# Performance work log

Measured on AMD Instinct MI355X. Metric: run time of the kernel, lower is better.

The kernel has to match this reference:

```python
import jax, jax.numpy as jnp
import numpy as np

N_NODES = 100000
N_EDGES = 1600000
D_IN, D_HID, D_OUT = 128, 128, 40


def _degrees(src, dst, n):
    ones = jnp.ones((src.shape[0],), dtype=jnp.float32)
    out_deg = jax.ops.segment_sum(ones, src, num_segments=n)
    in_deg = jax.ops.segment_sum(ones, dst, num_segments=n)
    # DGL clamps zero degrees to 1 to avoid inf
    return jnp.maximum(out_deg, 1.0), jnp.maximum(in_deg, 1.0)


def _graph_conv(x, W, b, src, dst, out_norm, in_norm, n):
    # norm='both': h = D_in^{-1/2} * A^T * (D_out^{-1/2} * x W) + b
    h = x @ W                      # [N, d_out] (W applied first: d_in >= d_out)
    h = h * out_norm[:, None]      # scale source features
    agg = jax.ops.segment_sum(h[src], dst, num_segments=n)  # gather-scatter SpMM
    return agg * in_norm[:, None] + b


def setup_inputs() -> dict:
    key = jax.random.key(0)
    ks = jax.random.split(key, 8)
    x = jax.random.normal(ks[0], (N_NODES, D_IN), dtype=jnp.float32)
    edge_index = jax.random.randint(ks[1], (2, N_EDGES), 0, N_NODES, dtype=jnp.int32)
    def glorot(k, fan_in, fan_out):
        lim = np.sqrt(6.0 / (fan_in + fan_out)).astype(np.float32)
        return jax.random.uniform(k, (fan_in, fan_out), jnp.float32, -lim, lim)
    return {
        "x": x,
        "edge_index": edge_index,
        "W1": glorot(ks[2], D_IN, D_HID), "b1": jnp.zeros((D_HID,), jnp.float32),
        "W2": glorot(ks[3], D_HID, D_HID), "b2": jnp.zeros((D_HID,), jnp.float32),
        "W3": glorot(ks[4], D_HID, D_OUT), "b3": jnp.zeros((D_OUT,), jnp.float32),
    }


def reference(x, edge_index, W1, b1, W2, b2, W3, b3):
    src, dst = edge_index[0], edge_index[1]
    out_deg, in_deg = _degrees(src, dst, N_NODES)
    out_norm = jax.lax.rsqrt(out_deg)
    in_norm = jax.lax.rsqrt(in_deg)
    h = _graph_conv(x, W1, b1, src, dst, out_norm, in_norm, N_NODES)
    h = jax.nn.relu(h)  # dropout inactive at inference
    h = _graph_conv(h, W2, b2, src, dst, out_norm, in_norm, N_NODES)
    h = jax.nn.relu(h)
    h = _graph_conv(h, W3, b3, src, dst, out_norm, in_norm, N_NODES)
    return jax.nn.log_softmax(h, axis=-1)
```

## Files before the change

kernel.cpp:

```cpp
#include <hip/hip_runtime.h>
#include <hip/hip_bf16.h>
#include <math.h>

typedef __hip_bfloat16 bf16;
typedef __attribute__((ext_vector_type(8))) short short8v;
typedef __attribute__((ext_vector_type(4))) float f32x4;

#define ELLW 64
#define NPB 256
#define NBMAX 512
#define CAPB 8192
#define CHUNKA 4096

__device__ __forceinline__ float bflo(unsigned u) { return __uint_as_float(u << 16); }
__device__ __forceinline__ float bfhi(unsigned u) { return __uint_as_float(u & 0xffff0000u); }
__device__ __forceinline__ unsigned short f2bf(float f) {
    unsigned u = __float_as_uint(f);
    return (unsigned short)((u + 0x7fff + ((u >> 16) & 1)) >> 16);
}


__device__ __forceinline__ void pack_one(const float* __restrict__ W, bf16* __restrict__ Wb,
                                         int idx, int NOUT, int NPAD) {
    int r = idx & 7;
    int rest = idx >> 3;
    int col = rest % NPAD;
    int sk = rest / NPAD;
    int k = sk * 8 + r;
    float v = (col < NOUT) ? W[k * NOUT + col] : 0.0f;
    Wb[idx] = __float2bfloat16(v);
}

__global__ void pack_all(const float* __restrict__ W1, const float* __restrict__ W2,
                         const float* __restrict__ W3, bf16* __restrict__ Wb1,
                         bf16* __restrict__ Wb2, bf16* __restrict__ Wb3) {
    int idx = blockIdx.x * blockDim.x + threadIdx.x;
    if (idx < 16384) pack_one(W1, Wb1, idx, 128, 128);
    else if (idx < 32768) pack_one(W2, Wb2, idx - 16384, 128, 128);
    else if (idx < 40960) pack_one(W3, Wb3, idx - 32768, 40, 64);
}


template <int NT>
__device__ void gemm_body_f32(int bid, const float* __restrict__ Af,
                              const bf16* __restrict__ Wb, bf16* __restrict__ H, int n) {
    constexpr int NPAD = NT * 16;
    int lane = threadIdx.x & 63;
    int wid = threadIdx.x >> 6;
    int base = (bid * 4 + wid) * 16;
    if (base >= n) return;
    int m = lane & 15, kb = lane >> 4;
    int arow = base + m;

    short8v az = {0, 0, 0, 0, 0, 0, 0, 0};
    short8v a[4];
    const float4* apf = (const float4*)(Af + (size_t)arow * 128);
#pragma unroll
    for (int s = 0; s < 4; ++s) {
        short8v w = az;
        if (arow < n) {
            float4 p = apf[s * 8 + kb * 2];
            float4 q = apf[s * 8 + kb * 2 + 1];
            w[0] = (short)f2bf(p.x); w[1] = (short)f2bf(p.y);
            w[2] = (short)f2bf(p.z); w[3] = (short)f2bf(p.w);
            w[4] = (short)f2bf(q.x); w[5] = (short)f2bf(q.y);
            w[6] = (short)f2bf(q.z); w[7] = (short)f2bf(q.w);
        }
        a[s] = w;
    }

    f32x4 zz = {0.f, 0.f, 0.f, 0.f};
    f32x4 acc[NT];
#pragma unroll
    for (int t = 0; t < NT; ++t) acc[t] = zz;

    const short8v* bp = (const short8v*)Wb;
#pragma unroll
    for (int s = 0; s < 4; ++s) {
#pragma unroll
        for (int t = 0; t < NT; ++t) {
            short8v b = bp[(size_t)(s * 4 + kb) * NPAD + t * 16 + m];
            acc[t] = __builtin_amdgcn_mfma_f32_16x16x32_bf16(a[s], b, acc[t], 0, 0, 0);
        }
    }

    int orow0 = base + kb * 4;
#pragma unroll
    for (int r = 0; r < 4; ++r) {
        int rr = orow0 + r;
        if (rr < n) {
#pragma unroll
            for (int t = 0; t < NT; ++t)
                H[(size_t)rr * NPAD + t * 16 + m] = __float2bfloat16(acc[t][r]);
        }
    }
}


__device__ void scatter_body(int bid, const int* __restrict__ src, const int* __restrict__ dst,
                             int nbk, int* __restrict__ gCurD, int* __restrict__ gCurS,
                             unsigned* __restrict__ pairD, int* __restrict__ srcS, int E) {
    __shared__ int histD[NBMAX], histS[NBMAX], offD[NBMAX], offS[NBMAX];
    int tid = threadIdx.x;
    int base = bid * CHUNKA;
    int cnt = E - base; if (cnt > CHUNKA) cnt = CHUNKA;
    for (int i = tid; i < nbk; i += 256) { histD[i] = 0; histS[i] = 0; }
    __syncthreads();
    int sv[16], dv[16];
#pragma unroll
    for (int j = 0; j < 16; ++j) {
        int idx = tid + j * 256;
        if (idx < cnt) {
            sv[j] = src[base + idx];
            dv[j] = dst[base + idx];
            atomicAdd(&histD[dv[j] >> 8], 1);
            atomicAdd(&histS[sv[j] >> 8], 1);
        } else sv[j] = -1;
    }
    __syncthreads();
    for (int i = tid; i < nbk; i += 256) {
        offD[i] = atomicAdd(&gCurD[i], histD[i]);
        offS[i] = atomicAdd(&gCurS[i], histS[i]);
    }
    __syncthreads();
    for (int i = tid; i < nbk; i += 256) { histD[i] = 0; histS[i] = 0; }
    __syncthreads();
#pragma unroll
    for (int j = 0; j < 16; ++j) {
        if (sv[j] >= 0) {
            int bd = dv[j] >> 8;
            int p = atomicAdd(&histD[bd], 1) + offD[bd];
            if (p < CAPB)
                pairD[(size_t)bd * CAPB + p] = ((unsigned)(dv[j] & 255) << 17) | (unsigned)sv[j];
            int bs = sv[j] >> 8;
            int q = atomicAdd(&histS[bs], 1) + offS[bs];
            if (q < CAPB) srcS[(size_t)bs * CAPB + q] = sv[j];
        }
    }
}


__global__ void phase1(const int* __restrict__ src, const int* __restrict__ dst,
                       int nbk, int* __restrict__ gCurD, int* __restrict__ gCurS,
                       unsigned* __restrict__ pairD, int* __restrict__ srcS, int E,
                       int scatterBlocks, const float* __restrict__ x,
                       const bf16* __restrict__ Wb1, bf16* __restrict__ H, int n) {
    if ((int)blockIdx.x < scatterBlocks)
        scatter_body(blockIdx.x, src, dst, nbk, gCurD, gCurS, pairD, srcS, E);
    else
        gemm_body_f32<8>(blockIdx.x - scatterBlocks, x, Wb1, H, n);
}


__global__ void phase2(const unsigned* __restrict__ pairD, const int* __restrict__ srcS,
                       const int* __restrict__ gCurD, const int* __restrict__ gCurS,
                       int* __restrict__ ell, int* __restrict__ cnt_in,
                       float* __restrict__ innf, float* __restrict__ outn, int nbk, int n) {
    int bid = blockIdx.x;
    int tid = threadIdx.x;
    if (bid < nbk) {
        __shared__ int cnt[NPB];
        cnt[tid & (NPB - 1)] = 0;
        __syncthreads();
        int m = gCurD[bid]; if (m > CAPB) m = CAPB;
        const unsigned* p = pairD + (size_t)bid * CAPB;
        int nb0 = bid << 8;
        for (int i = tid; i < m; i += 256) {
            unsigned v = p[i];
            int local = (int)(v >> 17);
            int s = (int)(v & 0x1FFFF);
            int pos = atomicAdd(&cnt[local], 1);
            if (pos < ELLW) ell[((size_t)(nb0 + local) << 6) + pos] = s;
        }
        __syncthreads();
        int node = nb0 + tid;
        if (tid < NPB && node < n) {
            cnt_in[node] = cnt[tid];
            innf[node] = rsqrtf(fmaxf((float)cnt[tid], 1.0f));
        }
    } else {
        int b = bid - nbk;
        __shared__ int cnt2[NPB];
        cnt2[tid & (NPB - 1)] = 0;
        __syncthreads();
        int m = gCurS[b]; if (m > CAPB) m = CAPB;
        const int* p = srcS + (size_t)b * CAPB;
        int nb0 = b << 8;
        for (int i = tid; i < m; i += 256)
            atomicAdd(&cnt2[p[i] - nb0], 1);
        __syncthreads();
        int node = nb0 + tid;
        if (tid < NPB && node < n)
            outn[node] = rsqrtf(fmaxf((float)cnt2[tid], 1.0f));
    }
}


template <int NT>
__global__ void gather_gemm_fused(const bf16* __restrict__ h, const int* __restrict__ cnt_in,
                                  const int* __restrict__ ell, const float* __restrict__ outn,
                                  const float* __restrict__ inn, const float* __restrict__ bias,
                                  const bf16* __restrict__ Wb, bf16* __restrict__ H, int n) {
    constexpr int NPAD = NT * 16;
    constexpr int NTW = NT / 4;
    __shared__ short rows[16][136];
    int lane = threadIdx.x & 63;
    int wid = threadIdx.x >> 6;
    int nodeBase = blockIdx.x * 16;
    const unsigned* hu = (const unsigned*)h;

#pragma unroll
    for (int q = 0; q < 4; ++q) {
        int r = wid * 4 + q;
        int node = nodeBase + r;
        unsigned pk = 0;
        if (node < n) {
            int d = min(cnt_in[node], ELLW);
            const int4* row4 = (const int4*)(ell + ((size_t)node << 6));
            const int* row = (const int*)row4;
            float a0 = 0.f, a1 = 0.f, a2 = 0.f, a3 = 0.f;
            float a4 = 0.f, a5 = 0.f, a6 = 0.f, a7 = 0.f;
            int k = 0;
            for (; k + 7 < d; k += 8) {
                int kq = k >> 2;
                int4 q0 = row4[kq], q1 = row4[kq + 1];
                unsigned u0 = hu[((size_t)q0.x << 6) + lane];
                unsigned u1 = hu[((size_t)q0.y << 6) + lane];
                unsigned u2 = hu[((size_t)q0.z << 6) + lane];
                unsigned u3 = hu[((size_t)q0.w << 6) + lane];
                unsigned u4 = hu[((size_t)q1.x << 6) + lane];
                unsigned u5 = hu[((size_t)q1.y << 6) + lane];
                unsigned u6 = hu[((size_t)q1.z << 6) + lane];
                unsigned u7 = hu[((size_t)q1.w << 6) + lane];
                float o0 = outn[q0.x], o1 = outn[q0.y], o2 = outn[q0.z], o3 = outn[q0.w];
                float o4 = outn[q1.x], o5 = outn[q1.y], o6 = outn[q1.z], o7 = outn[q1.w];
                a0 += o0 * bflo(u0); a1 += o0 * bfhi(u0);
                a2 += o1 * bflo(u1); a3 += o1 * bfhi(u1);
                a4 += o2 * bflo(u2); a5 += o2 * bfhi(u2);
                a6 += o3 * bflo(u3); a7 += o3 * bfhi(u3);
                a0 += o4 * bflo(u4); a1 += o4 * bfhi(u4);
                a2 += o5 * bflo(u5); a3 += o5 * bfhi(u5);
                a4 += o6 * bflo(u6); a5 += o6 * bfhi(u6);
                a6 += o7 * bflo(u7); a7 += o7 * bfhi(u7);
            }
            for (; k + 3 < d; k += 4) {
                int4 q0 = row4[k >> 2];
                unsigned u0 = hu[((size_t)q0.x << 6) + lane];
                unsigned u1 = hu[((size_t)q0.y << 6) + lane];
                unsigned u2 = hu[((size_t)q0.z << 6) + lane];
                unsigned u3 = hu[((size_t)q0.w << 6) + lane];
                float o0 = outn[q0.x], o1 = outn[q0.y], o2 = outn[q0.z], o3 = outn[q0.w];
                a0 += o0 * bflo(u0); a1 += o0 * bfhi(u0);
                a2 += o1 * bflo(u1); a3 += o1 * bfhi(u1);
                a4 += o2 * bflo(u2); a5 += o2 * bfhi(u2);
                a6 += o3 * bflo(u3); a7 += o3 * bfhi(u3);
            }
            for (; k < d; ++k) {
                int e = row[k];
                unsigned u = hu[((size_t)e << 6) + lane];
                float o = outn[e];
                a0 += o * bflo(u); a1 += o * bfhi(u);
            }
            float innv = inn[node];
            float2 bb = ((const float2*)bias)[lane];
            float f0 = fmaxf(((a0 + a2) + (a4 + a6)) * innv + bb.x, 0.0f);
            float f1 = fmaxf(((a1 + a3) + (a5 + a7)) * innv + bb.y, 0.0f);
            pk = (unsigned)f2bf(f0) | ((unsigned)f2bf(f1) << 16);
        }
        ((unsigned*)rows[r])[lane] = pk;
    }
    __syncthreads();

    int m = lane & 15, kb = lane >> 4;
    short8v a[4];
#pragma unroll
    for (int s = 0; s < 4; ++s)
        a[s] = *(const short8v*)&rows[m][s * 32 + kb * 8];

    f32x4 zz = {0.f, 0.f, 0.f, 0.f};
    f32x4 acc[NTW];
#pragma unroll
    for (int t = 0; t < NTW; ++t) acc[t] = zz;

    const short8v* bp = (const short8v*)Wb;
#pragma unroll
    for (int s = 0; s < 4; ++s) {
#pragma unroll
        for (int t = 0; t < NTW; ++t) {
            int tt = wid * NTW + t;
            short8v b = bp[(size_t)(s * 4 + kb) * NPAD + tt * 16 + m];
            acc[t] = __builtin_amdgcn_mfma_f32_16x16x32_bf16(a[s], b, acc[t], 0, 0, 0);
        }
    }

    int orow0 = nodeBase + kb * 4;
#pragma unroll
    for (int r = 0; r < 4; ++r) {
        int rr = orow0 + r;
        if (rr < n) {
#pragma unroll
            for (int t = 0; t < NTW; ++t)
                H[(size_t)rr * NPAD + (wid * NTW + t) * 16 + m] = __float2bfloat16(acc[t][r]);
        }
    }
}


__global__ void gather40_lsm_p64(const bf16* __restrict__ h, const int* __restrict__ cnt_in,
                                 const int* __restrict__ ell, const float* __restrict__ outn,
                                 const float* __restrict__ inn, const float* __restrict__ b,
                                 float* __restrict__ out, int n) {
    int node = blockIdx.x * 4 + (threadIdx.x >> 6);
    int lane = threadIdx.x & 63;
    if (node >= n) return;
    int d = min(cnt_in[node], ELLW);
    const int* row = ell + ((size_t)node << 6);
    int grp = lane >> 5;
    int l = lane & 31;
    const unsigned* hu = (const unsigned*)h;
    float a0 = 0.f, a1 = 0.f, a2 = 0.f, a3 = 0.f;
    int k = grp;
    for (; k + 14 < d; k += 16) {
        int e0 = row[k],      e1 = row[k + 2],  e2 = row[k + 4],  e3 = row[k + 6];
        int e4 = row[k + 8],  e5 = row[k + 10], e6 = row[k + 12], e7 = row[k + 14];
        unsigned u0 = hu[((size_t)e0 << 5) + l];
        unsigned u1 = hu[((size_t)e1 << 5) + l];
        unsigned u2 = hu[((size_t)e2 << 5) + l];
        unsigned u3 = hu[((size_t)e3 << 5) + l];
        unsigned u4 = hu[((size_t)e4 << 5) + l];
        unsigned u5 = hu[((size_t)e5 << 5) + l];
        unsigned u6 = hu[((size_t)e6 << 5) + l];
        unsigned u7 = hu[((size_t)e7 << 5) + l];
        float o0 = outn[e0], o1 = outn[e1], o2 = outn[e2], o3 = outn[e3];
        float o4 = outn[e4], o5 = outn[e5], o6 = outn[e6], o7 = outn[e7];
        a0 += o0 * bflo(u0); a1 += o0 * bfhi(u0);
        a2 += o1 * bflo(u1); a3 += o1 * bfhi(u1);
        a0 += o2 * bflo(u2); a1 += o2 * bfhi(u2);
        a2 += o3 * bflo(u3); a3 += o3 * bfhi(u3);
        a0 += o4 * bflo(u4); a1 += o4 * bfhi(u4);
        a2 += o5 * bflo(u5); a3 += o5 * bfhi(u5);
        a0 += o6 * bflo(u6); a1 += o6 * bfhi(u6);
        a2 += o7 * bflo(u7); a3 += o7 * bfhi(u7);
    }
    for (; k + 6 < d; k += 8) {
        int e0 = row[k], e1 = row[k + 2], e2 = row[k + 4], e3 = row[k + 6];
        unsigned u0 = hu[((size_t)e0 << 5) + l];
        unsigned u1 = hu[((size_t)e1 << 5) + l];
        unsigned u2 = hu[((size_t)e2 << 5) + l];
        unsigned u3 = hu[((size_t)e3 << 5) + l];
        float o0 = outn[e0], o1 = outn[e1], o2 = outn[e2], o3 = outn[e3];
        a0 += o0 * bflo(u0); a1 += o0 * bfhi(u0);
        a2 += o1 * bflo(u1); a3 += o1 * bfhi(u1);
        a0 += o2 * bflo(u2); a1 += o2 * bfhi(u2);
        a2 += o3 * bflo(u3); a3 += o3 * bfhi(u3);
    }
    for (; k + 2 < d; k += 4) {
        int e0 = row[k], e1 = row[k + 2];
        unsigned u0 = hu[((size_t)e0 << 5) + l];
        unsigned u1 = hu[((size_t)e1 << 5) + l];
        float o0 = outn[e0], o1 = outn[e1];
        a0 += o0 * bflo(u0); a1 += o0 * bfhi(u0);
        a2 += o1 * bflo(u1); a3 += o1 * bfhi(u1);
    }
    if (k < d) {
        int e = row[k];
        unsigned u = hu[((size_t)e << 5) + l];
        float o = outn[e];
        a0 += o * bflo(u); a1 += o * bfhi(u);
    }
    a0 += a2; a1 += a3;
    a0 += __shfl_xor(a0, 32);
    a1 += __shfl_xor(a1, 32);
    float innv = inn[node];
    bool act = (l < 20);
    float2 bb = act ? ((const float2*)b)[l] : make_float2(0.f, 0.f);
    float v0 = act ? (a0 * innv + bb.x) : -INFINITY;
    float v1 = act ? (a1 * innv + bb.y) : -INFINITY;
    float m = fmaxf(v0, v1);
#pragma unroll
    for (int o = 16; o; o >>= 1) m = fmaxf(m, __shfl_xor(m, o));
    float e = act ? (expf(v0 - m) + expf(v1 - m)) : 0.0f;
#pragma unroll
    for (int o = 16; o; o >>= 1) e += __shfl_xor(e, o);
    float ls = m + logf(e);
    if (act && grp == 0)
        ((float2*)(out + (size_t)node * 40))[l] = make_float2(v0 - ls, v1 - ls);
}


extern "C" void kernel_launch(void* const* d_in, const int* in_sizes, int n_in,
                              void* d_out, int out_size, void* d_ws, size_t ws_size,
                              hipStream_t stream) {
    const float* x  = (const float*)d_in[0];
    const int*   ei = (const int*)d_in[1];
    const float* W1 = (const float*)d_in[2];
    const float* b1 = (const float*)d_in[3];
    const float* W2 = (const float*)d_in[4];
    const float* b2 = (const float*)d_in[5];
    const float* W3 = (const float*)d_in[6];
    const float* b3 = (const float*)d_in[7];

    const int n = in_sizes[0] / 128;
    const int E = in_sizes[1] / 2;
    const int* src = ei;
    const int* dst = ei + E;
    const int nbk = (n + NPB - 1) / NPB;

    char* wsb = (char*)d_ws;
    size_t off = 0;
    auto alloc = [&](size_t bytes) { void* p = wsb + off; off = (off + bytes + 63) & ~(size_t)63; return p; };
    float*    outn    = (float*)alloc((size_t)n * 4);
    float*    innf    = (float*)alloc((size_t)n * 4);
    int*      cnt_in  = (int*)alloc((size_t)n * 4);
    int*      gCurD   = (int*)alloc((size_t)nbk * 4);
    int*      gCurS   = (int*)alloc((size_t)nbk * 4);
    int*      ell     = (int*)alloc((size_t)n * ELLW * 4);
    unsigned* pairD   = (unsigned*)alloc((size_t)nbk * CAPB * 4);
    bf16*     Wb1     = (bf16*)alloc(16 * 128 * 8 * 2);
    bf16*     Wb2     = (bf16*)alloc(16 * 128 * 8 * 2);
    bf16*     Wb3     = (bf16*)alloc(16 * 64 * 8 * 2);
    bf16*     hb      = (bf16*)alloc((size_t)n * 128 * 2);
    bf16*     gb      = (bf16*)alloc((size_t)n * 128 * 2);
    int*      srcS    = (int*)gb;

    hipMemsetAsync(gCurD, 0, ((size_t)((char*)gCurS - (char*)gCurD) + (size_t)nbk * 4), stream);

    pack_all<<<(40960 + 255) / 256, 256, 0, stream>>>(W1, W2, W3, Wb1, Wb2, Wb3);

    const int scatterBlocks = (E + CHUNKA - 1) / CHUNKA;
    const int gemmBlocks = (n + 63) / 64;
    phase1<<<scatterBlocks + gemmBlocks, 256, 0, stream>>>(src, dst, nbk, gCurD, gCurS, pairD,
                                                           srcS, E, scatterBlocks, x, Wb1, hb, n);
    phase2<<<2 * nbk, 256, 0, stream>>>(pairD, srcS, gCurD, gCurS, ell, cnt_in, innf, outn,
                                        nbk, n);

    const int fblk = (n + 15) / 16;
    gather_gemm_fused<8><<<fblk, 256, 0, stream>>>(hb, cnt_in, ell, outn, innf, b1, Wb2, gb, n);
    gather_gemm_fused<4><<<fblk, 256, 0, stream>>>(gb, cnt_in, ell, outn, innf, b2, Wb3, hb, n);
    gather40_lsm_p64<<<(n + 3) / 4, 256, 0, stream>>>(hb, cnt_in, ell, outn, innf, b3,
                                                      (float*)d_out, n);
}
```

Measured before the change: 270.3 us.

## Fold source out-degree norm into GEMM epilogue and vectorize edge scatter

Layers 2 and 3 now multiply each row by its out-degree norm in the GEMM epilogue before storing it, so their gathers drop the per-edge outn load and multiply. Layer 1 still gathers outn per edge because its input comes from the phase1 GEMM, which is unchanged. The scatter phase doubles its chunk size and reads src/dst as int4 instead of holding 16 values per thread in registers. The NT=4 GEMM also exits idle waves early. The cost is an extra rounding point, since the norm is applied before the bf16 store, and fewer scatter blocks with more work each.

```diff
diff --git a/kernel.cpp b/kernel.cpp
--- a/kernel.cpp
+++ b/kernel.cpp
@@ -10,7 +10,7 @@
 #define NPB 256
 #define NBMAX 512
 #define CAPB 8192
-#define CHUNKA 4096
+#define CHUNKA 8192
 
 __device__ __forceinline__ float bflo(unsigned u) { return __uint_as_float(u << 16); }
 __device__ __forceinline__ float bfhi(unsigned u) { return __uint_as_float(u & 0xffff0000u); }
@@ -106,16 +106,22 @@
     int cnt = E - base; if (cnt > CHUNKA) cnt = CHUNKA;
     for (int i = tid; i < nbk; i += 256) { histD[i] = 0; histS[i] = 0; }
     __syncthreads();
-    int sv[16], dv[16];
-#pragma unroll
-    for (int j = 0; j < 16; ++j) {
-        int idx = tid + j * 256;
-        if (idx < cnt) {
-            sv[j] = src[base + idx];
-            dv[j] = dst[base + idx];
-            atomicAdd(&histD[dv[j] >> 8], 1);
-            atomicAdd(&histS[sv[j] >> 8], 1);
-        } else sv[j] = -1;
+#pragma unroll
+    for (int j = 0; j < CHUNKA / 1024; ++j) {
+        int i0 = (j * 256 + tid) * 4;
+        if (i0 + 3 < cnt) {
+            int4 s4 = *(const int4*)(src + base + i0);
+            int4 d4 = *(const int4*)(dst + base + i0);
+            atomicAdd(&histD[d4.x >> 8], 1); atomicAdd(&histS[s4.x >> 8], 1);
+            atomicAdd(&histD[d4.y >> 8], 1); atomicAdd(&histS[s4.y >> 8], 1);
+            atomicAdd(&histD[d4.z >> 8], 1); atomicAdd(&histS[s4.z >> 8], 1);
+            atomicAdd(&histD[d4.w >> 8], 1); atomicAdd(&histS[s4.w >> 8], 1);
+        } else {
+            for (int i = i0; i < cnt && i < i0 + 4; ++i) {
+                atomicAdd(&histD[dst[base + i] >> 8], 1);
+                atomicAdd(&histS[src[base + i] >> 8], 1);
+            }
+        }
     }
     __syncthreads();
     for (int i = tid; i < nbk; i += 256) {
@@ -126,15 +132,28 @@
     for (int i = tid; i < nbk; i += 256) { histD[i] = 0; histS[i] = 0; }
     __syncthreads();
 #pragma unroll
-    for (int j = 0; j < 16; ++j) {
-        if (sv[j] >= 0) {
-            int bd = dv[j] >> 8;
-            int p = atomicAdd(&histD[bd], 1) + offD[bd];
-            if (p < CAPB)
-                pairD[(size_t)bd * CAPB + p] = ((unsigned)(dv[j] & 255) << 17) | (unsigned)sv[j];
-            int bs = sv[j] >> 8;
-            int q = atomicAdd(&histS[bs], 1) + offS[bs];
-            if (q < CAPB) srcS[(size_t)bs * CAPB + q] = sv[j];
+    for (int j = 0; j < CHUNKA / 1024; ++j) {
+        int i0 = (j * 256 + tid) * 4;
+        int lim = cnt - i0; if (lim > 4) lim = 4;
+        if (lim > 0) {
+            int ss[4], dd[4];
+            if (lim == 4) {
+                int4 s4 = *(const int4*)(src + base + i0);
+                int4 d4 = *(const int4*)(dst + base + i0);
+                ss[0] = s4.x; ss[1] = s4.y; ss[2] = s4.z; ss[3] = s4.w;
+                dd[0] = d4.x; dd[1] = d4.y; dd[2] = d4.z; dd[3] = d4.w;
+            } else {
+                for (int i = 0; i < lim; ++i) { ss[i] = src[base + i0 + i]; dd[i] = dst[base + i0 + i]; }
+            }
+            for (int i = 0; i < lim; ++i) {
+                int bd = dd[i] >> 8;
+                int p = atomicAdd(&histD[bd], 1) + offD[bd];
+                if (p < CAPB)
+                    pairD[(size_t)bd * CAPB + p] = ((unsigned)(dd[i] & 255) << 17) | (unsigned)ss[i];
+                int bs = ss[i] >> 8;
+                int q = atomicAdd(&histS[bs], 1) + offS[bs];
+                if (q < CAPB) srcS[(size_t)bs * CAPB + q] = ss[i];
+            }
         }
     }
 }
@@ -196,7 +215,7 @@
 }
 
 
-template <int NT>
+template <int NT, bool EDGE_OUTN>
 __global__ void gather_gemm_fused(const bf16* __restrict__ h, const int* __restrict__ cnt_in,
                                   const int* __restrict__ ell, const float* __restrict__ outn,
                                   const float* __restrict__ inn, const float* __restrict__ bias,
@@ -232,16 +251,27 @@
                 unsigned u5 = hu[((size_t)q1.y << 6) + lane];
                 unsigned u6 = hu[((size_t)q1.z << 6) + lane];
                 unsigned u7 = hu[((size_t)q1.w << 6) + lane];
-                float o0 = outn[q0.x], o1 = outn[q0.y], o2 = outn[q0.z], o3 = outn[q0.w];
-                float o4 = outn[q1.x], o5 = outn[q1.y], o6 = outn[q1.z], o7 = outn[q1.w];
-                a0 += o0 * bflo(u0); a1 += o0 * bfhi(u0);
-                a2 += o1 * bflo(u1); a3 += o1 * bfhi(u1);
-                a4 += o2 * bflo(u2); a5 += o2 * bfhi(u2);
-                a6 += o3 * bflo(u3); a7 += o3 * bfhi(u3);
-                a0 += o4 * bflo(u4); a1 += o4 * bfhi(u4);
-                a2 += o5 * bflo(u5); a3 += o5 * bfhi(u5);
-                a4 += o6 * bflo(u6); a5 += o6 * bfhi(u6);
-                a6 += o7 * bflo(u7); a7 += o7 * bfhi(u7);
+                if constexpr (EDGE_OUTN) {
+                    float o0 = outn[q0.x], o1 = outn[q0.y], o2 = outn[q0.z], o3 = outn[q0.w];
+                    float o4 = outn[q1.x], o5 = outn[q1.y], o6 = outn[q1.z], o7 = outn[q1.w];
+                    a0 += o0 * bflo(u0); a1 += o0 * bfhi(u0);
+                    a2 += o1 * bflo(u1); a3 += o1 * bfhi(u1);
+                    a4 += o2 * bflo(u2); a5 += o2 * bfhi(u2);
+                    a6 += o3 * bflo(u3); a7 += o3 * bfhi(u3);
+                    a0 += o4 * bflo(u4); a1 += o4 * bfhi(u4);
+                    a2 += o5 * bflo(u5); a3 += o5 * bfhi(u5);
+                    a4 += o6 * bflo(u6); a5 += o6 * bfhi(u6);
+                    a6 += o7 * bflo(u7); a7 += o7 * bfhi(u7);
+                } else {
+                    a0 += bflo(u0); a1 += bfhi(u0);
+                    a2 += bflo(u1); a3 += bfhi(u1);
+                    a4 += bflo(u2); a5 += bfhi(u2);
+                    a6 += bflo(u3); a7 += bfhi(u3);
+                    a0 += bflo(u4); a1 += bfhi(u4);
+                    a2 += bflo(u5); a3 += bfhi(u5);
+                    a4 += bflo(u6); a5 += bfhi(u6);
+                    a6 += bflo(u7); a7 += bfhi(u7);
+                }
             }
             for (; k + 3 < d; k += 4) {
                 int4 q0 = row4[k >> 2];
@@ -249,17 +279,28 @@
                 unsigned u1 = hu[((size_t)q0.y << 6) + lane];
                 unsigned u2 = hu[((size_t)q0.z << 6) + lane];
                 unsigned u3 = hu[((size_t)q0.w << 6) + lane];
-                float o0 = outn[q0.x], o1 = outn[q0.y], o2 = outn[q0.z], o3 = outn[q0.w];
-                a0 += o0 * bflo(u0); a1 += o0 * bfhi(u0);
-                a2 += o1 * bflo(u1); a3 += o1 * bfhi(u1);
-                a4 += o2 * bflo(u2); a5 += o2 * bfhi(u2);
-                a6 += o3 * bflo(u3); a7 += o3 * bfhi(u3);
+                if constexpr (EDGE_OUTN) {
+                    float o0 = outn[q0.x], o1 = outn[q0.y], o2 = outn[q0.z], o3 = outn[q0.w];
+                    a0 += o0 * bflo(u0); a1 += o0 * bfhi(u0);
+                    a2 += o1 * bflo(u1); a3 += o1 * bfhi(u1);
+                    a4 += o2 * bflo(u2); a5 += o2 * bfhi(u2);
+                    a6 += o3 * bflo(u3); a7 += o3 * bfhi(u3);
+                } else {
+                    a0 += bflo(u0); a1 += bfhi(u0);
+                    a2 += bflo(u1); a3 += bfhi(u1);
+                    a4 += bflo(u2); a5 += bfhi(u2);
+                    a6 += bflo(u3); a7 += bfhi(u3);
+                }
             }
             for (; k < d; ++k) {
                 int e = row[k];
                 unsigned u = hu[((size_t)e << 6) + lane];
-                float o = outn[e];
-                a0 += o * bflo(u); a1 += o * bfhi(u);
+                if constexpr (EDGE_OUTN) {
+                    float o = outn[e];
+                    a0 += o * bflo(u); a1 += o * bfhi(u);
+                } else {
+                    a0 += bflo(u); a1 += bfhi(u);
+                }
             }
             float innv = inn[node];
             float2 bb = ((const float2*)bias)[lane];
@@ -271,6 +312,7 @@
     }
     __syncthreads();
 
+    if (NT == 4 && wid == 3) return;
     int m = lane & 15, kb = lane >> 4;
     short8v a[4];
 #pragma unroll
@@ -298,16 +340,17 @@
     for (int r = 0; r < 4; ++r) {
         int rr = orow0 + r;
         if (rr < n) {
+            float sc = outn[rr];
 #pragma unroll
             for (int t = 0; t < NTW; ++t)
-                H[(size_t)rr * NPAD + (wid * NTW + t) * 16 + m] = __float2bfloat16(acc[t][r]);
+                H[(size_t)rr * NPAD + (wid * NTW + t) * 16 + m] = __float2bfloat16(acc[t][r] * sc);
         }
     }
 }
 
 
 __global__ void gather40_lsm_p64(const bf16* __restrict__ h, const int* __restrict__ cnt_in,
-                                 const int* __restrict__ ell, const float* __restrict__ outn,
+                                 const int* __restrict__ ell,
                                  const float* __restrict__ inn, const float* __restrict__ b,
                                  float* __restrict__ out, int n) {
     int node = blockIdx.x * 4 + (threadIdx.x >> 6);
@@ -331,16 +374,14 @@
         unsigned u5 = hu[((size_t)e5 << 5) + l];
         unsigned u6 = hu[((size_t)e6 << 5) + l];
         unsigned u7 = hu[((size_t)e7 << 5) + l];
-        float o0 = outn[e0], o1 = outn[e1], o2 = outn[e2], o3 = outn[e3];
-        float o4 = outn[e4], o5 = outn[e5], o6 = outn[e6], o7 = outn[e7];
-        a0 += o0 * bflo(u0); a1 += o0 * bfhi(u0);
-        a2 += o1 * bflo(u1); a3 += o1 * bfhi(u1);
-        a0 += o2 * bflo(u2); a1 += o2 * bfhi(u2);
-        a2 += o3 * bflo(u3); a3 += o3 * bfhi(u3);
-        a0 += o4 * bflo(u4); a1 += o4 * bfhi(u4);
-        a2 += o5 * bflo(u5); a3 += o5 * bfhi(u5);
-        a0 += o6 * bflo(u6); a1 += o6 * bfhi(u6);
-        a2 += o7 * bflo(u7); a3 += o7 * bfhi(u7);
+        a0 += bflo(u0); a1 += bfhi(u0);
+        a2 += bflo(u1); a3 += bfhi(u1);
+        a0 += bflo(u2); a1 += bfhi(u2);
+        a2 += bflo(u3); a3 += bfhi(u3);
+        a0 += bflo(u4); a1 += bfhi(u4);
+        a2 += bflo(u5); a3 += bfhi(u5);
+        a0 += bflo(u6); a1 += bfhi(u6);
+        a2 += bflo(u7); a3 += bfhi(u7);
     }
     for (; k + 6 < d; k += 8) {
         int e0 = row[k], e1 = row[k + 2], e2 = row[k + 4], e3 = row[k + 6];
@@ -348,25 +389,22 @@
         unsigned u1 = hu[((size_t)e1 << 5) + l];
         unsigned u2 = hu[((size_t)e2 << 5) + l];
         unsigned u3 = hu[((size_t)e3 << 5) + l];
-        float o0 = outn[e0], o1 = outn[e1], o2 = outn[e2], o3 = outn[e3];
-        a0 += o0 * bflo(u0); a1 += o0 * bfhi(u0);
-        a2 += o1 * bflo(u1); a3 += o1 * bfhi(u1);
-        a0 += o2 * bflo(u2); a1 += o2 * bfhi(u2);
-        a2 += o3 * bflo(u3); a3 += o3 * bfhi(u3);
+        a0 += bflo(u0); a1 += bfhi(u0);
+        a2 += bflo(u1); a3 += bfhi(u1);
+        a0 += bflo(u2); a1 += bfhi(u2);
+        a2 += bflo(u3); a3 += bfhi(u3);
     }
     for (; k + 2 < d; k += 4) {
         int e0 = row[k], e1 = row[k + 2];
         unsigned u0 = hu[((size_t)e0 << 5) + l];
         unsigned u1 = hu[((size_t)e1 << 5) + l];
-        float o0 = outn[e0], o1 = outn[e1];
-        a0 += o0 * bflo(u0); a1 += o0 * bfhi(u0);
-        a2 += o1 * bflo(u1); a3 += o1 * bfhi(u1);
+        a0 += bflo(u0); a1 += bfhi(u0);
+        a2 += bflo(u1); a3 += bfhi(u1);
     }
     if (k < d) {
         int e = row[k];
         unsigned u = hu[((size_t)e << 5) + l];
-        float o = outn[e];
-        a0 += o * bflo(u); a1 += o * bfhi(u);
+        a0 += bflo(u); a1 += bfhi(u);
     }
     a0 += a2; a1 += a3;
     a0 += __shfl_xor(a0, 32);
@@ -435,8 +473,10 @@
                                         nbk, n);
 
     const int fblk = (n + 15) / 16;
-    gather_gemm_fused<8><<<fblk, 256, 0, stream>>>(hb, cnt_in, ell, outn, innf, b1, Wb2, gb, n);
-    gather_gemm_fused<4><<<fblk, 256, 0, stream>>>(gb, cnt_in, ell, outn, innf, b2, Wb3, hb, n);
-    gather40_lsm_p64<<<(n + 3) / 4, 256, 0, stream>>>(hb, cnt_in, ell, outn, innf, b3,
+    gather_gemm_fused<8, true><<<fblk, 256, 0, stream>>>(hb, cnt_in, ell, outn, innf, b1,
+                                                         Wb2, gb, n);
+    gather_gemm_fused<4, false><<<fblk, 256, 0, stream>>>(gb, cnt_in, ell, outn, innf, b2,
+                                                          Wb3, hb, n);
+    gather40_lsm_p64<<<(n + 3) / 4, 256, 0, stream>>>(hb, cnt_in, ell, innf, b3,
                                                       (float*)d_out, n);
 }
```

Measured after the change: 263.5 us (median of 2 runs). 2.5% less time.
